# Kernel tuning notes

Hardware: AMD Instinct MI355X
Metric: run time of the kernel (lower is better)

## Reference

```python
import jax, jax.numpy as jnp
import numpy as np


def _bilinear_gather(img, y, x):
    """Bilinear sample img [B,C,H,W] at float coords y,x [B,K,H,W] with zero padding.
    Returns [B,C,K,H,W]."""
    B, C, H, W = img.shape
    K = y.shape[1]
    y0 = jnp.floor(y)
    x0 = jnp.floor(x)
    wy = y - y0  # fractional weights [B,K,H,W]
    wx = x - x0
    y0i = y0.astype(jnp.int32)
    x0i = x0.astype(jnp.int32)
    flat = img.reshape(B, C, 1, H * W)

    def gather(yi, xi):
        valid = (yi >= 0) & (yi < H) & (xi >= 0) & (xi < W)  # [B,K,H,W]
        idx = jnp.clip(yi, 0, H - 1) * W + jnp.clip(xi, 0, W - 1)
        v = jnp.take_along_axis(flat, idx.reshape(B, 1, K, H * W), axis=-1)
        v = v.reshape(B, C, K, H, W)
        return v * valid[:, None].astype(img.dtype)

    v00 = gather(y0i, x0i)
    v01 = gather(y0i, x0i + 1)
    v10 = gather(y0i + 1, x0i)
    v11 = gather(y0i + 1, x0i + 1)
    wy_ = wy[:, None]  # [B,1,K,H,W]
    wx_ = wx[:, None]
    return (v00 * (1 - wy_) * (1 - wx_) + v01 * (1 - wy_) * wx_
            + v10 * wy_ * (1 - wx_) + v11 * wy_ * wx_)


def deform_conv2d(inp, offsets, ker):
    """torchvision.ops.deform_conv2d with stride=1, dilation=1, padding=k//2, groups=1."""
    B, C, H, W = inp.shape
    Co, Ci, k, _ = ker.shape
    pad = k // 2
    K = k * k
    off = offsets.reshape(B, K, 2, H, W)
    dy = off[:, :, 0]  # [B,K,H,W] (y offset first per torchvision convention)
    dx = off[:, :, 1]
    ii, jj = jnp.meshgrid(jnp.arange(k), jnp.arange(k), indexing='ij')
    ky = ii.reshape(K).astype(inp.dtype)  # kernel tap row index
    kx = jj.reshape(K).astype(inp.dtype)
    hgrid = jnp.arange(H, dtype=inp.dtype)
    wgrid = jnp.arange(W, dtype=inp.dtype)
    # sampling coords: p = out_pos - pad + tap + offset
    y = dy + (hgrid[None, None, :, None] - pad) + ky[None, :, None, None]
    x = dx + (wgrid[None, None, None, :] - pad) + kx[None, :, None, None]
    sampled = _bilinear_gather(inp, y, x)  # [B,C,K,H,W]
    return jnp.einsum('bckhw,ock->bohw', sampled, ker.reshape(Co, Ci, K))


def setup_inputs() -> dict:
    key = jax.random.key(0)
    k1, k2, k3, k4 = jax.random.split(key, 4)
    B, C, H, W, Co, k = 4, 16, 256, 256, 16, 3
    offsets = jax.random.normal(k1, (B, 2 * k * k, H, W), dtype=jnp.float32)
    inp = jax.random.normal(k2, (B, C, H, W), dtype=jnp.float32)
    ker = jax.random.normal(k3, (Co, C, k, k), dtype=jnp.float32) * 0.1
    target = jax.random.normal(k4, (B, Co, H, W), dtype=jnp.float32)
    return {"offsets": offsets, "input": inp, "ker": ker, "target": target}


def reference(offsets, input, ker, target):
    deformed = deform_conv2d(input, offsets, ker)
    # criterion = MSELoss (mean reduction)
    loss = jnp.mean((deformed - target) ** 2)
    return loss
```

## Files before the change

kernel.cpp:

```cpp
#include <hip/hip_runtime.h>

#define B_  4
#define C_  16
#define H_  256
#define W_  256
#define CO_ 16
#define KS_ 3
#define KK_ 9
#define HW_ (H_ * W_)
#define IMG_WORDS ((size_t)B_ * HW_ * 8)
#define KER_OFF   IMG_WORDS
#define NKB 5
#define NBLK 4096
#define PART_OFF (KER_OFF + (size_t)NKB * 256)

typedef __attribute__((ext_vector_type(8))) short bf16x8;
typedef __attribute__((ext_vector_type(4))) float f32x4;
union U4S8 { uint4 u; bf16x8 s; };

#define LOBF(u) __uint_as_float((u) << 16)
#define HIBF(u) __uint_as_float((u) & 0xffff0000u)

__device__ __forceinline__ unsigned rne_bf16(float v) {
    unsigned b = __float_as_uint(v);
    return (b + 0x7fffu + ((b >> 16) & 1u)) >> 16;
}

__global__ __launch_bounds__(256) void pack_nhwc_bf16(
    const float* __restrict__ inp, const float* __restrict__ ker,
    unsigned* __restrict__ wsu)
{
    const int t = threadIdx.x;
    const int e = blockIdx.x * 256 + t;
    const int b = e >> 16;
    const int hw = e & (HW_ - 1);
    const float* src = inp + (size_t)b * (C_ * HW_) + hw;
    float v[C_];
#pragma unroll
    for (int c = 0; c < C_; c++)
        v[c] = src[c * HW_];
    unsigned u[8];
#pragma unroll
    for (int j = 0; j < 8; j++)
        u[j] = rne_bf16(v[2 * j]) | (rne_bf16(v[2 * j + 1]) << 16);
    uint4* dst = ((uint4*)wsu) + (size_t)e * 2;
    dst[0] = make_uint4(u[0], u[1], u[2], u[3]);
    dst[1] = make_uint4(u[4], u[5], u[6], u[7]);

    if (blockIdx.x == 0) {
        for (int i = t; i < NKB * 256; i += 256) {
            const int wj  = i & 3;
            const int l   = (i >> 2) & 63;
            const int blk = i >> 8;
            const int o   = l & 15;
            unsigned lo = 0, hi = 0;
            {
                int j = 2 * wj, k = (l >> 4) * 8 + j;
                int tap = 2 * blk + (k >> 4), c = k & 15;
                if (tap <= 8) lo = rne_bf16(ker[(o * C_ + c) * KK_ + tap]);
                j = 2 * wj + 1; k = (l >> 4) * 8 + j;
                tap = 2 * blk + (k >> 4); c = k & 15;
                if (tap <= 8) hi = rne_bf16(ker[(o * C_ + c) * KK_ + tap]);
            }
            wsu[KER_OFF + i] = lo | (hi << 16);
        }
    }
}

__device__ __forceinline__ void tap_setup(
    int h, int w, int kk, float dy, float dx,
    int* idx, float* wt)
{
    const float y = dy + (float)(h - 1 + kk / KS_);
    const float x = dx + (float)(w - 1 + kk % KS_);
    const float y0f = floorf(y);
    const float x0f = floorf(x);
    const int   y0  = (int)y0f;
    const int   x0  = (int)x0f;
    const float wy  = y - y0f;
    const float wx  = x - x0f;

    float w00 = (1.f - wy) * (1.f - wx);
    float w01 = (1.f - wy) * wx;
    float w10 = wy * (1.f - wx);
    float w11 = wy * wx;

    const bool v0y = ((unsigned)y0       < (unsigned)H_);
    const bool v1y = ((unsigned)(y0 + 1) < (unsigned)H_);
    const bool v0x = ((unsigned)x0       < (unsigned)W_);
    const bool v1x = ((unsigned)(x0 + 1) < (unsigned)W_);

    wt[0] = (v0y & v0x) ? w00 : 0.f;
    wt[1] = (v0y & v1x) ? w01 : 0.f;
    wt[2] = (v1y & v0x) ? w10 : 0.f;
    wt[3] = (v1y & v1x) ? w11 : 0.f;

    const int y0c = min(max(y0,     0), H_ - 1);
    const int y1c = min(max(y0 + 1, 0), H_ - 1);
    const int x0c = min(max(x0,     0), W_ - 1);
    const int x1c = min(max(x0 + 1, 0), W_ - 1);

    idx[0] = y0c * W_ + x0c;
    idx[1] = y0c * W_ + x1c;
    idx[2] = y1c * W_ + x0c;
    idx[3] = y1c * W_ + x1c;
}

__device__ __forceinline__ unsigned blendpack(
    unsigned a, unsigned b, unsigned c, unsigned d,
    float w0, float w1, float w2, float w3)
{
    const float lo = w0 * LOBF(a) + w1 * LOBF(b) + w2 * LOBF(c) + w3 * LOBF(d);
    const float hi = w0 * HIBF(a) + w1 * HIBF(b) + w2 * HIBF(c) + w3 * HIBF(d);
    return rne_bf16(lo) | (rne_bf16(hi) << 16);
}

__global__ __launch_bounds__(256) void deform_loss_mfma(
    const float* __restrict__ off, const unsigned* __restrict__ wsu,
    const float* __restrict__ tgt, float* __restrict__ partials)
{
    const int f = (blockIdx.x & 7) * 512 + (blockIdx.x >> 3);
    const int t = threadIdx.x;
    const int l = t & 63;
    const int q = l >> 4;
    const int m = l & 15;
    const int base = f * 64 + (t >> 6) * 16;
    const int pix  = base + m;
    const int b    = pix >> 16;
    const int hw   = pix & (HW_ - 1);
    const int h    = hw >> 8;
    const int w    = hw & (W_ - 1);

    const float* offb = off + (size_t)b * (2 * KK_ * HW_) + hw;
    const uint4* ib   = ((const uint4*)wsu) + (size_t)b * HW_ * 2;
    const uint4* kb   = (const uint4*)(wsu + KER_OFF);

    bf16x8 bfr[NKB];
#pragma unroll
    for (int kbk = 0; kbk < NKB; kbk++) {
        U4S8 cv; cv.u = kb[kbk * 64 + l];
        bfr[kbk] = cv.s;
    }

    float dyv[NKB], dxv[NKB];
#pragma unroll
    for (int kbk = 0; kbk < NKB; kbk++) {
        const int tap = min(2 * kbk + (q >> 1), KK_ - 1);
        dyv[kbk] = offb[(2 * tap) * HW_];
        dxv[kbk] = offb[(2 * tap + 1) * HW_];
    }

    f32x4 acc = {0.f, 0.f, 0.f, 0.f};
    uint4 cor[2][4];
    float wts[2][4];

    {
        int idx[4];
        tap_setup(h, w, min(q >> 1, KK_ - 1), dyv[0], dxv[0], idx, wts[0]);
#pragma unroll
        for (int i = 0; i < 4; i++) cor[0][i] = ib[idx[i] * 2 + (q & 1)];
    }

#pragma unroll
    for (int kbk = 0; kbk < NKB; kbk++) {
        const int cur = kbk & 1, nxt = cur ^ 1;
        if (kbk + 1 < NKB) {
            int idx[4];
            tap_setup(h, w, min(2 * (kbk + 1) + (q >> 1), KK_ - 1),
                      dyv[kbk + 1], dxv[kbk + 1], idx, wts[nxt]);
#pragma unroll
            for (int i = 0; i < 4; i++) cor[nxt][i] = ib[idx[i] * 2 + (q & 1)];
        }

        const float w0 = wts[cur][0], w1 = wts[cur][1],
                    w2 = wts[cur][2], w3 = wts[cur][3];
        const uint4 c0 = cor[cur][0], c1 = cor[cur][1],
                    c2 = cor[cur][2], c3 = cor[cur][3];
        uint4 A4;
        A4.x = blendpack(c0.x, c1.x, c2.x, c3.x, w0, w1, w2, w3);
        A4.y = blendpack(c0.y, c1.y, c2.y, c3.y, w0, w1, w2, w3);
        A4.z = blendpack(c0.z, c1.z, c2.z, c3.z, w0, w1, w2, w3);
        A4.w = blendpack(c0.w, c1.w, c2.w, c3.w, w0, w1, w2, w3);
        U4S8 ca; ca.u = A4;

        acc = __builtin_amdgcn_mfma_f32_16x16x32_bf16(ca.s, bfr[kbk], acc, 0, 0, 0);
    }

    const int o   = m;
    const int hwb = (base & (HW_ - 1)) + 4 * q;
    const float4 tv = *(const float4*)(tgt + (size_t)b * (CO_ * HW_)
                                       + (size_t)o * HW_ + hwb);
    float d0 = acc[0] - tv.x, d1 = acc[1] - tv.y,
          d2 = acc[2] - tv.z, d3 = acc[3] - tv.w;
    float part = (d0 * d0 + d1 * d1 + d2 * d2 + d3 * d3)
               * (1.0f / (float)((size_t)B_ * CO_ * HW_));

#pragma unroll
    for (int sft = 32; sft > 0; sft >>= 1)
        part += __shfl_down(part, sft, 64);

    __shared__ float red[4];
    if (l == 0)
        red[t >> 6] = part;
    __syncthreads();
    if (t == 0)
        partials[blockIdx.x] = red[0] + red[1] + red[2] + red[3];
}

__global__ __launch_bounds__(256) void reduce_partials(
    const float* __restrict__ partials, float* __restrict__ out)
{
    const int t = threadIdx.x;
    float s = 0.f;
#pragma unroll
    for (int i = 0; i < NBLK / 256; i++)
        s += partials[t + i * 256];
#pragma unroll
    for (int sft = 32; sft > 0; sft >>= 1)
        s += __shfl_down(s, sft, 64);
    __shared__ float red[4];
    if ((t & 63) == 0) red[t >> 6] = s;
    __syncthreads();
    if (t == 0) out[0] = red[0] + red[1] + red[2] + red[3];
}

__global__ __launch_bounds__(256) void deform_loss_kernel(
    const float* __restrict__ off, const float* __restrict__ inp,
    const float* __restrict__ ker, const float* __restrict__ tgt,
    float* __restrict__ out)
{
    const int idx = blockIdx.x * blockDim.x + threadIdx.x;
    float part = 0.f;
    if (idx < B_ * H_ * W_) {
        const int w  = idx & (W_ - 1);
        const int h  = (idx >> 8) & (H_ - 1);
        const int b  = idx >> 16;
        const int hw = h * W_ + w;
        const float* offb = off + (size_t)b * (2 * KK_ * HW_);
        const float* inpb = inp + (size_t)b * (C_ * HW_);
        float acc[CO_];
#pragma unroll
        for (int o = 0; o < CO_; o++) acc[o] = 0.f;
        for (int kk = 0; kk < KK_; kk++) {
            const float dy = offb[(2 * kk)     * HW_ + hw];
            const float dx = offb[(2 * kk + 1) * HW_ + hw];
            const float y = dy + (float)(h - 1 + kk / KS_);
            const float x = dx + (float)(w - 1 + kk % KS_);
            const float y0f = floorf(y);
            const float x0f = floorf(x);
            const int   y0  = (int)y0f;
            const int   x0  = (int)x0f;
            const float wy  = y - y0f;
            const float wx  = x - x0f;
            float w00 = (1.f - wy) * (1.f - wx);
            float w01 = (1.f - wy) * wx;
            float w10 = wy * (1.f - wx);
            float w11 = wy * wx;
            const bool v0y = ((unsigned)y0       < (unsigned)H_);
            const bool v1y = ((unsigned)(y0 + 1) < (unsigned)H_);
            const bool v0x = ((unsigned)x0       < (unsigned)W_);
            const bool v1x = ((unsigned)(x0 + 1) < (unsigned)W_);
            w00 = (v0y & v0x) ? w00 : 0.f;
            w01 = (v0y & v1x) ? w01 : 0.f;
            w10 = (v1y & v0x) ? w10 : 0.f;
            w11 = (v1y & v1x) ? w11 : 0.f;
            const int i00 = min(max(y0,0),H_-1)*W_ + min(max(x0,0),W_-1);
            const int i01 = min(max(y0,0),H_-1)*W_ + min(max(x0+1,0),W_-1);
            const int i10 = min(max(y0+1,0),H_-1)*W_ + min(max(x0,0),W_-1);
            const int i11 = min(max(y0+1,0),H_-1)*W_ + min(max(x0+1,0),W_-1);
            for (int c = 0; c < C_; c++) {
                const float* pp = inpb + c * HW_;
                const float s = pp[i00]*w00 + pp[i01]*w01 + pp[i10]*w10 + pp[i11]*w11;
#pragma unroll
                for (int o = 0; o < CO_; o++)
                    acc[o] = fmaf(s, ker[(o * C_ + c) * KK_ + kk], acc[o]);
            }
        }
        const float* tb = tgt + (size_t)b * (CO_ * HW_);
#pragma unroll
        for (int o = 0; o < CO_; o++) {
            const float d = acc[o] - tb[o * HW_ + hw];
            part = fmaf(d, d, part);
        }
        part *= (1.0f / (float)((size_t)B_ * CO_ * HW_));
    }
#pragma unroll
    for (int sft = 32; sft > 0; sft >>= 1)
        part += __shfl_down(part, sft, 64);
    if ((threadIdx.x & 63) == 0)
        atomicAdd(out, part);
}

extern "C" void kernel_launch(void* const* d_in, const int* in_sizes, int n_in,
                              void* d_out, int out_size, void* d_ws, size_t ws_size,
                              hipStream_t stream) {
    const float* offsets = (const float*)d_in[0];
    const float* input   = (const float*)d_in[1];
    const float* ker     = (const float*)d_in[2];
    const float* target  = (const float*)d_in[3];
    float* out = (float*)d_out;

    const size_t need = (PART_OFF + NBLK) * sizeof(unsigned);
    if (ws_size >= need) {
        unsigned* wsu = (unsigned*)d_ws;
        pack_nhwc_bf16<<<(B_ * HW_) / 256, 256, 0, stream>>>(input, ker, wsu);
        deform_loss_mfma<<<NBLK, 256, 0, stream>>>(
            offsets, wsu, target, (float*)(wsu + PART_OFF));
        reduce_partials<<<1, 256, 0, stream>>>(
            (const float*)(wsu + PART_OFF), out);
    } else {
        hipMemsetAsync(out, 0, sizeof(float), stream);
        const int total = B_ * H_ * W_;
        deform_loss_kernel<<<(total + 255) / 256, 256, 0, stream>>>(
            offsets, input, ker, target, out);
    }
}
```

Measured before the change: 115.7 us.

## Process two 16-pixel groups per wave and truncate bf16 packing via perm

Each wave now handles 32 pixels as two MFMA tiles, halving the block count and spreading the kernel-fragment loads and the per-block reduction over twice as much work. The offset and target loads are issued up front for both groups, and the gather pipeline runs across 10 MFMA steps. The bf16 packing switches from round-to-nearest-even to a single byte-permute truncation, which saves ALU work at some cost in accuracy.

```diff
diff --git a/kernel.cpp b/kernel.cpp
--- a/kernel.cpp
+++ b/kernel.cpp
@@ -11,7 +11,7 @@
 #define IMG_WORDS ((size_t)B_ * HW_ * 8)
 #define KER_OFF   IMG_WORDS
 #define NKB 5
-#define NBLK 4096
+#define NBLK 2048
 #define PART_OFF (KER_OFF + (size_t)NKB * 256)
 
 typedef __attribute__((ext_vector_type(8))) short bf16x8;
@@ -112,26 +112,26 @@
 {
     const float lo = w0 * LOBF(a) + w1 * LOBF(b) + w2 * LOBF(c) + w3 * LOBF(d);
     const float hi = w0 * HIBF(a) + w1 * HIBF(b) + w2 * HIBF(c) + w3 * HIBF(d);
-    return rne_bf16(lo) | (rne_bf16(hi) << 16);
+    return __builtin_amdgcn_perm(__float_as_uint(hi), __float_as_uint(lo),
+                                 0x07060302u);
 }
 
 __global__ __launch_bounds__(256) void deform_loss_mfma(
     const float* __restrict__ off, const unsigned* __restrict__ wsu,
     const float* __restrict__ tgt, float* __restrict__ partials)
 {
-    const int f = (blockIdx.x & 7) * 512 + (blockIdx.x >> 3);
+    const int f = (blockIdx.x & 7) * 256 + (blockIdx.x >> 3);
     const int t = threadIdx.x;
     const int l = t & 63;
     const int q = l >> 4;
     const int m = l & 15;
-    const int base = f * 64 + (t >> 6) * 16;
-    const int pix  = base + m;
-    const int b    = pix >> 16;
-    const int hw   = pix & (HW_ - 1);
-    const int h    = hw >> 8;
-    const int w    = hw & (W_ - 1);
-
-    const float* offb = off + (size_t)b * (2 * KK_ * HW_) + hw;
+    const int base = f * 128 + (t >> 6) * 32;
+    const int b    = base >> 16;
+    const int hwb  = base & (HW_ - 1);
+    const int h    = hwb >> 8;
+    const int w0   = (hwb & (W_ - 1)) + m;
+
+    const float* offp = off + (size_t)b * (2 * KK_ * HW_) + (size_t)h * W_;
     const uint4* ib   = ((const uint4*)wsu) + (size_t)b * HW_ * 2;
     const uint4* kb   = (const uint4*)(wsu + KER_OFF);
 
@@ -142,57 +142,65 @@
         bfr[kbk] = cv.s;
     }
 
-    float dyv[NKB], dxv[NKB];
-#pragma unroll
-    for (int kbk = 0; kbk < NKB; kbk++) {
-        const int tap = min(2 * kbk + (q >> 1), KK_ - 1);
-        dyv[kbk] = offb[(2 * tap) * HW_];
-        dxv[kbk] = offb[(2 * tap + 1) * HW_];
-    }
-
-    f32x4 acc = {0.f, 0.f, 0.f, 0.f};
+    float dyv[2][NKB], dxv[2][NKB];
+#pragma unroll
+    for (int g = 0; g < 2; g++)
+#pragma unroll
+        for (int kbk = 0; kbk < NKB; kbk++) {
+            const int tap = min(2 * kbk + (q >> 1), KK_ - 1);
+            dyv[g][kbk] = offp[(size_t)(2 * tap) * HW_ + w0 + 16 * g];
+            dxv[g][kbk] = offp[(size_t)(2 * tap + 1) * HW_ + w0 + 16 * g];
+        }
+    const float* tbase = tgt + (size_t)b * (CO_ * HW_) + (size_t)m * HW_
+                       + hwb + 4 * q;
+    const float4 tv0 = *(const float4*)(tbase);
+    const float4 tv1 = *(const float4*)(tbase + 16);
+
+    f32x4 acc[2] = {{0.f, 0.f, 0.f, 0.f}, {0.f, 0.f, 0.f, 0.f}};
     uint4 cor[2][4];
     float wts[2][4];
 
     {
         int idx[4];
-        tap_setup(h, w, min(q >> 1, KK_ - 1), dyv[0], dxv[0], idx, wts[0]);
+        tap_setup(h, w0, min(q >> 1, KK_ - 1), dyv[0][0], dxv[0][0], idx, wts[0]);
 #pragma unroll
         for (int i = 0; i < 4; i++) cor[0][i] = ib[idx[i] * 2 + (q & 1)];
     }
 
 #pragma unroll
-    for (int kbk = 0; kbk < NKB; kbk++) {
-        const int cur = kbk & 1, nxt = cur ^ 1;
-        if (kbk + 1 < NKB) {
+    for (int kbi = 0; kbi < 2 * NKB; kbi++) {
+        const int cur = kbi & 1, nxt = cur ^ 1;
+        if (kbi + 1 < 2 * NKB) {
+            const int gn = (kbi + 1) / NKB, kn = (kbi + 1) % NKB;
             int idx[4];
-            tap_setup(h, w, min(2 * (kbk + 1) + (q >> 1), KK_ - 1),
-                      dyv[kbk + 1], dxv[kbk + 1], idx, wts[nxt]);
+            tap_setup(h, w0 + 16 * gn, min(2 * kn + (q >> 1), KK_ - 1),
+                      dyv[gn][kn], dxv[gn][kn], idx, wts[nxt]);
 #pragma unroll
             for (int i = 0; i < 4; i++) cor[nxt][i] = ib[idx[i] * 2 + (q & 1)];
         }
 
-        const float w0 = wts[cur][0], w1 = wts[cur][1],
-                    w2 = wts[cur][2], w3 = wts[cur][3];
+        const int g = kbi / NKB, kkb = kbi % NKB;
+        const float w0_ = wts[cur][0], w1_ = wts[cur][1],
+                    w2_ = wts[cur][2], w3_ = wts[cur][3];
         const uint4 c0 = cor[cur][0], c1 = cor[cur][1],
                     c2 = cor[cur][2], c3 = cor[cur][3];
         uint4 A4;
-        A4.x = blendpack(c0.x, c1.x, c2.x, c3.x, w0, w1, w2, w3);
-        A4.y = blendpack(c0.y, c1.y, c2.y, c3.y, w0, w1, w2, w3);
-        A4.z = blendpack(c0.z, c1.z, c2.z, c3.z, w0, w1, w2, w3);
-        A4.w = blendpack(c0.w, c1.w, c2.w, c3.w, w0, w1, w2, w3);
+        A4.x = blendpack(c0.x, c1.x, c2.x, c3.x, w0_, w1_, w2_, w3_);
+        A4.y = blendpack(c0.y, c1.y, c2.y, c3.y, w0_, w1_, w2_, w3_);
+        A4.z = blendpack(c0.z, c1.z, c2.z, c3.z, w0_, w1_, w2_, w3_);
+        A4.w = blendpack(c0.w, c1.w, c2.w, c3.w, w0_, w1_, w2_, w3_);
         U4S8 ca; ca.u = A4;
 
-        acc = __builtin_amdgcn_mfma_f32_16x16x32_bf16(ca.s, bfr[kbk], acc, 0, 0, 0);
-    }
-
-    const int o   = m;
-    const int hwb = (base & (HW_ - 1)) + 4 * q;
-    const float4 tv = *(const float4*)(tgt + (size_t)b * (CO_ * HW_)
-                                       + (size_t)o * HW_ + hwb);
-    float d0 = acc[0] - tv.x, d1 = acc[1] - tv.y,
-          d2 = acc[2] - tv.z, d3 = acc[3] - tv.w;
-    float part = (d0 * d0 + d1 * d1 + d2 * d2 + d3 * d3)
+        acc[g] = __builtin_amdgcn_mfma_f32_16x16x32_bf16(ca.s, bfr[kkb],
+                                                         acc[g], 0, 0, 0);
+    }
+
+    float d0 = acc[0][0] - tv0.x, d1 = acc[0][1] - tv0.y,
+          d2 = acc[0][2] - tv0.z, d3 = acc[0][3] - tv0.w;
+    float e0 = acc[1][0] - tv1.x, e1 = acc[1][1] - tv1.y,
+          e2 = acc[1][2] - tv1.z, e3 = acc[1][3] - tv1.w;
+    float part = (d0 * d0 + d1 * d1 + d2 * d2 + d3 * d3
+                + e0 * e0 + e1 * e1 + e2 * e2 + e3 * e3)
                * (1.0f / (float)((size_t)B_ * CO_ * HW_));
 
 #pragma unroll
```

After: 113.8 us, median of 2. Within noise of the previous version (-1.6%).
